# Kernel optimization log

Measured on AMD Instinct MI355X. Metric: run time of the kernel, lower is better.

The kernel has to match this reference:

```python
import jax, jax.numpy as jnp
import numpy as np

B, D, C, P, H, I, E, TOPK = 65536, 1024, 256, 32, 128, 32, 16, 2
FUSION = D + P  # 1056

def ln(x, g, b, eps=1e-5):
    m = jnp.mean(x, axis=-1, keepdims=True)
    v = jnp.mean((x - m) ** 2, axis=-1, keepdims=True)
    return (x - m) * jax.lax.rsqrt(v + eps) * g + b

def setup_inputs() -> dict:
    key = jax.random.key(0)
    ks = jax.random.split(key, 8)
    def w(k, shape):
        return jax.random.normal(k, shape, dtype=jnp.float32) * 0.02
    return {
        "x": jax.random.normal(ks[0], (B, D), dtype=jnp.float32),
        "context": jax.random.normal(ks[1], (B, C), dtype=jnp.float32),
        "en_g": jnp.ones((D,), jnp.float32), "en_b": jnp.zeros((D,), jnp.float32),
        "cn_g": jnp.ones((C,), jnp.float32), "cn_b": jnp.zeros((C,), jnp.float32),
        "cp1_w": w(ks[2], (C, P)), "cp1_b": jnp.zeros((P,), jnp.float32),
        "cp2_w": w(ks[3], (P, P)), "cp2_b": jnp.zeros((P,), jnp.float32),
        "cpn_g": jnp.ones((P,), jnp.float32), "cpn_b": jnp.zeros((P,), jnp.float32),
        "fn_g": jnp.ones((FUSION,), jnp.float32), "fn_b": jnp.zeros((FUSION,), jnp.float32),
        "gp1_w": w(ks[4], (FUSION, H)), "gp1_b": jnp.zeros((H,), jnp.float32),
        "ln1_g": jnp.ones((H,), jnp.float32), "ln1_b": jnp.zeros((H,), jnp.float32),
        "gp2_w": w(ks[5], (H, I)), "gp2_b": jnp.zeros((I,), jnp.float32),
        "ln2_g": jnp.ones((I,), jnp.float32), "ln2_b": jnp.zeros((I,), jnp.float32),
        "gp3_w": w(ks[6], (I, E)), "gp3_b": jnp.zeros((E,), jnp.float32),
    }

def reference(x, context, en_g, en_b, cn_g, cn_b, cp1_w, cp1_b, cp2_w, cp2_b,
              cpn_g, cpn_b, fn_g, fn_b, gp1_w, gp1_b, ln1_g, ln1_b,
              gp2_w, gp2_b, ln2_g, ln2_b, gp3_w, gp3_b):
    gelu = lambda t: jax.nn.gelu(t, approximate=False)  # torch default GELU (erf)
    emb = ln(x, en_g, en_b)                               # [B, D]
    ctx = ln(context, cn_g, cn_b)                         # [B, C]
    cf = gelu(ctx @ cp1_w + cp1_b) @ cp2_w + cp2_b        # [B, P]
    cf = ln(cf, cpn_g, cpn_b)
    fusion = ln(jnp.concatenate([emb, cf], axis=-1), fn_g, fn_b)  # [B, FUSION]
    h = gelu(ln(fusion @ gp1_w + gp1_b, ln1_g, ln1_b))    # [B, H]
    inter = gelu(ln(h @ gp2_w + gp2_b, ln2_g, ln2_b))     # [B, I]
    clean_logits = inter @ gp3_w + gp3_b                  # [B, E]
    # inference path: no noise injection (training=False)
    top_v, top_i = jax.lax.top_k(clean_logits, TOPK)
    combined_weights = jax.nn.softmax(top_v / 1.0, axis=-1)  # temperature=1.0
    return combined_weights, top_i, clean_logits
```

## Files before the change

### kernel.cpp

```cpp
#include <hip/hip_runtime.h>
#include <math.h>

namespace {

using s8v = __attribute__((ext_vector_type(8))) short;
using vf4 = __attribute__((ext_vector_type(4))) float;

constexpr int Bn = 65536;
constexpr int Rn = 64;

constexpr size_t OFF_A1H  = 0;
constexpr size_t OFF_A1M  = 270336;
constexpr size_t OFF_A1L  = 540672;
constexpr size_t OFF_C1H  = 811008;
constexpr size_t OFF_C1M  = 827392;
constexpr size_t OFF_C1L  = 843776;
constexpr size_t OFF_C2H  = 860160;
constexpr size_t OFF_C2M  = 862208;
constexpr size_t OFF_C2L  = 864256;
constexpr size_t OFF_G2H  = 866304;
constexpr size_t OFF_G2M  = 874496;
constexpr size_t OFF_G2L  = 882688;
constexpr size_t OFF_VPK  = 890880;
constexpr size_t OFF_UPK  = 892928;
constexpr size_t OFF_CST  = 893184;
constexpr size_t OFF_VPART= 893216;

__device__ __forceinline__ unsigned short bf16_rn(float f) {
    unsigned u = __float_as_uint(f);
    u += 0x7FFFu + ((u >> 16) & 1u);
    return (unsigned short)(u >> 16);
}
__device__ __forceinline__ float bf16_tof(unsigned short h) {
    return __uint_as_float(((unsigned)h) << 16);
}

union S8U { s8v v; unsigned short u[8]; };
union S8P { s8v v; unsigned u32[4]; };

__device__ __forceinline__ vf4 MFMA(s8v a, s8v b, vf4 c) {
    return __builtin_amdgcn_mfma_f32_16x16x32_bf16(a, b, c, 0, 0, 0);
}

__device__ __forceinline__ void mfma6(vf4& acc, s8v ah, s8v am, s8v al,
                                      s8v bh, s8v bm, s8v bl) {
    acc = MFMA(ah, bh, acc);
    acc = MFMA(ah, bm, acc);
    acc = MFMA(am, bh, acc);
    acc = MFMA(ah, bl, acc);
    acc = MFMA(al, bh, acc);
    acc = MFMA(am, bm, acc);
}

__device__ __forceinline__ void split3(float v, unsigned short& h,
                                       unsigned short& m, unsigned short& l) {
    h = bf16_rn(v);
    const float r = v - bf16_tof(h);
    m = bf16_rn(r);
    const float r2 = r - bf16_tof(m);
    l = bf16_rn(r2);
}

__device__ __forceinline__ void split3x8(const float* vv, s8v& H, s8v& M, s8v& L) {
    S8P h, m, l;
    #pragma unroll
    for (int p = 0; p < 4; ++p) {
        const float lo = vv[2 * p], hi = vv[2 * p + 1];
        unsigned ph, pm, pl;
        asm("v_cvt_pk_bf16_f32 %0, %1, %2" : "=v"(ph) : "v"(lo), "v"(hi));
        const float rlo = lo - __uint_as_float(ph << 16);
        const float rhi = hi - __uint_as_float(ph & 0xFFFF0000u);
        asm("v_cvt_pk_bf16_f32 %0, %1, %2" : "=v"(pm) : "v"(rlo), "v"(rhi));
        const float slo = rlo - __uint_as_float(pm << 16);
        const float shi = rhi - __uint_as_float(pm & 0xFFFF0000u);
        asm("v_cvt_pk_bf16_f32 %0, %1, %2" : "=v"(pl) : "v"(slo), "v"(shi));
        h.u32[p] = ph; m.u32[p] = pm; l.u32[p] = pl;
    }
    H = h.v; M = m.v; L = l.v;
}

__device__ __forceinline__ float gelu_f(float v) {
    return 0.5f * v * (1.0f + erff(v * 0.70710678118654752440f));
}

__device__ __forceinline__ void red16(float& s) {
    s += __shfl_xor(s, 1, 64); s += __shfl_xor(s, 2, 64);
    s += __shfl_xor(s, 4, 64); s += __shfl_xor(s, 8, 64);
}

__global__ void cag_prek1(const float* __restrict__ gp1_w,
                          const float* __restrict__ en_g, const float* __restrict__ en_b,
                          const float* __restrict__ fn_g, const float* __restrict__ fn_b,
                          char* __restrict__ ws)
{
    const int t = threadIdx.x, ch = blockIdx.x;
    s8v* A1h = (s8v*)(ws + OFF_A1H);
    s8v* A1m = (s8v*)(ws + OFF_A1M);
    s8v* A1l = (s8v*)(ws + OFF_A1L);
    float* Vpart = (float*)(ws + OFF_VPART);

    for (int s = t; s < 512; s += 256) {
        const int nt = s >> 6, lane = s & 63;
        const int n = nt * 16 + (lane & 15);
        const int jb = ch * 32 + 8 * (lane >> 4);
        S8U h, m, lo;
        #pragma unroll
        for (int r = 0; r < 8; ++r) {
            const int j = jb + r;
            const float sc = fn_g[j] * (j < 1024 ? en_g[j] : 1.0f);
            const float a = sc * gp1_w[(size_t)j * 128 + n];
            split3(a, h.u[r], m.u[r], lo.u[r]);
        }
        A1h[(ch * 8 + nt) * 64 + lane] = h.v;
        A1m[(ch * 8 + nt) * 64 + lane] = m.v;
        A1l[(ch * 8 + nt) * 64 + lane] = lo.v;
    }
    if (t < 128) {
        float v1 = 0.f, v2 = 0.f, v3 = 0.f, v4 = 0.f;
        for (int jj = 0; jj < 32; ++jj) {
            const int j = ch * 32 + jj;
            const float wv = gp1_w[(size_t)j * 128 + t];
            const float fg = fn_g[j];
            if (j < 1024) { v1 = fmaf(fg * en_g[j], wv, v1); v2 = fmaf(fg * en_b[j], wv, v2); }
            v3 = fmaf(fg, wv, v3);
            v4 = fmaf(fn_b[j], wv, v4);
        }
        float* p = Vpart + ((size_t)ch * 128 + t) * 4;
        p[0] = v1; p[1] = v2; p[2] = v3; p[3] = v4;
    }
}

__global__ void cag_prek2(const float* __restrict__ en_g, const float* __restrict__ en_b,
                          const float* __restrict__ cn_g, const float* __restrict__ cn_b,
                          const float* __restrict__ cp1_w, const float* __restrict__ cp1_b,
                          const float* __restrict__ cp2_w, const float* __restrict__ gp2_w,
                          const float* __restrict__ gp1_b,
                          char* __restrict__ ws)
{
    const int t = threadIdx.x, b = blockIdx.x;
    if (b == 0) {
        const float* Vpart = (const float*)(ws + OFF_VPART);
        float* Vpk = (float*)(ws + OFF_VPK);
        float* cst = (float*)(ws + OFF_CST);
        if (t < 128) {
            float v1 = 0.f, v2 = 0.f, v3 = 0.f, v4 = 0.f;
            for (int ch = 0; ch < 33; ++ch) {
                const float* p = Vpart + ((size_t)ch * 128 + t) * 4;
                v1 += p[0]; v2 += p[1]; v3 += p[2]; v4 += p[3];
            }
            v4 += gp1_b[t];
            float* q = Vpk + t * 4;
            q[0] = v1; q[1] = v2; q[2] = v3; q[3] = v4;
        }
        __shared__ float red[256];
        float part[5] = {0.f, 0.f, 0.f, 0.f, 0.f};
        for (int i = t; i < 1024; i += 256) {
            const float g = en_g[i], bb = en_b[i];
            part[0] += g; part[1] += bb; part[2] += g * g; part[3] += g * bb; part[4] += bb * bb;
        }
        for (int f = 0; f < 5; ++f) {
            red[t] = part[f]; __syncthreads();
            for (int s = 128; s > 0; s >>= 1) { if (t < s) red[t] += red[t + s]; __syncthreads(); }
            if (t == 0) cst[f] = red[0];
            __syncthreads();
        }
    } else if (b == 1) {
        s8v* C1h = (s8v*)(ws + OFF_C1H);
        s8v* C1m = (s8v*)(ws + OFF_C1M);
        s8v* C1l = (s8v*)(ws + OFF_C1L);
        float* up = (float*)(ws + OFF_UPK);
        for (int s = t; s < 8 * 2 * 64; s += 256) {
            const int ks = s >> 7, nt = (s >> 6) & 1, lane = s & 63;
            const int n = nt * 16 + (lane & 15);
            const int kb = ks * 32 + 8 * (lane >> 4);
            S8U h, m, lo;
            #pragma unroll
            for (int r = 0; r < 8; ++r) {
                const int k = kb + r;
                const float a = cn_g[k] * cp1_w[k * 32 + n];
                split3(a, h.u[r], m.u[r], lo.u[r]);
            }
            C1h[(ks * 2 + nt) * 64 + lane] = h.v;
            C1m[(ks * 2 + nt) * 64 + lane] = m.v;
            C1l[(ks * 2 + nt) * 64 + lane] = lo.v;
        }
        if (t < 32) {
            float u1 = 0.f, u2 = 0.f;
            for (int c = 0; c < 256; ++c) {
                u1 = fmaf(cn_g[c], cp1_w[c * 32 + t], u1);
                u2 = fmaf(cn_b[c], cp1_w[c * 32 + t], u2);
            }
            up[2 * t] = u1; up[2 * t + 1] = u2 + cp1_b[t];
        }
    } else if (b == 2) {
        s8v* C2h = (s8v*)(ws + OFF_C2H);
        s8v* C2m = (s8v*)(ws + OFF_C2M);
        s8v* C2l = (s8v*)(ws + OFF_C2L);
        if (t < 128) {
            const int nt = t >> 6, lane = t & 63;
            const int n = nt * 16 + (lane & 15);
            const int kb = 8 * (lane >> 4);
            S8U h, m, lo;
            #pragma unroll
            for (int r = 0; r < 8; ++r) {
                const float a = cp2_w[(kb + r) * 32 + n];
                split3(a, h.u[r], m.u[r], lo.u[r]);
            }
            C2h[nt * 64 + lane] = h.v;
            C2m[nt * 64 + lane] = m.v;
            C2l[nt * 64 + lane] = lo.v;
        }
    } else {
        s8v* G2h = (s8v*)(ws + OFF_G2H);
        s8v* G2m = (s8v*)(ws + OFF_G2M);
        s8v* G2l = (s8v*)(ws + OFF_G2L);
        for (int s = t; s < 4 * 2 * 64; s += 256) {
            const int ks = s >> 7, nt = (s >> 6) & 1, lane = s & 63;
            const int n = nt * 16 + (lane & 15);
            const int kb = ks * 32 + 8 * (lane >> 4);
            S8U h, m, lo;
            #pragma unroll
            for (int r = 0; r < 8; ++r) {
                const float a = gp2_w[(kb + r) * 32 + n];
                split3(a, h.u[r], m.u[r], lo.u[r]);
            }
            G2h[(ks * 2 + nt) * 64 + lane] = h.v;
            G2m[(ks * 2 + nt) * 64 + lane] = m.v;
            G2l[(ks * 2 + nt) * 64 + lane] = lo.v;
        }
    }
}

__global__ __launch_bounds__(256, 4)
void cag_main(const float* __restrict__ x, const float* __restrict__ ctx,
              const float* __restrict__ en_g, const float* __restrict__ en_b,
              const float* __restrict__ cpn_g, const float* __restrict__ cpn_b,
              const float* __restrict__ cp2_b,
              const float* __restrict__ ln1_g, const float* __restrict__ ln1_b,
              const float* __restrict__ gp2_b,
              const float* __restrict__ ln2_g, const float* __restrict__ ln2_b,
              const float* __restrict__ gp3_w, const float* __restrict__ gp3_b,
              const char* __restrict__ ws, float* __restrict__ out)
{
    __shared__ __attribute__((aligned(16))) char smU[64 * 132 * 4];
    __shared__ float s_sc4[64][4];
    __shared__ float part_s[4][64];
    __shared__ float part_s2[4][64];
    __shared__ float s_ln1[64][2];
    __shared__ float s_cfs[64], s_cfs2[64];

    short (*fragA)[4][64][8] = (short(*)[4][64][8])smU;
    float (*cfnbuf)[36] = (float(*)[36])(smU + 12288);
    float (*pbuf)[36]   = (float(*)[36])smU;
    float (*hbuf)[132]  = (float(*)[132])smU;
    float (*ibuf)[36]   = (float(*)[36])smU;
    float (*lbuf)[20]   = (float(*)[20])(smU + 16384);

    const int tid = threadIdx.x;
    const int l = tid & 63, w = tid >> 6;
    const int sg = l >> 4, lr = l & 15;
    const int row0 = blockIdx.x * Rn;

    const s8v* A1h = (const s8v*)(ws + OFF_A1H);
    const s8v* A1m = (const s8v*)(ws + OFF_A1M);
    const s8v* A1l = (const s8v*)(ws + OFF_A1L);
    const s8v* C1h = (const s8v*)(ws + OFF_C1H);
    const s8v* C1m = (const s8v*)(ws + OFF_C1M);
    const s8v* C1l = (const s8v*)(ws + OFF_C1L);
    const s8v* C2h = (const s8v*)(ws + OFF_C2H);
    const s8v* C2m = (const s8v*)(ws + OFF_C2M);
    const s8v* C2l = (const s8v*)(ws + OFF_C2L);
    const s8v* G2h = (const s8v*)(ws + OFF_G2H);
    const s8v* G2m = (const s8v*)(ws + OFF_G2M);
    const s8v* G2l = (const s8v*)(ws + OFF_G2L);
    const float* Vpk = (const float*)(ws + OFF_VPK);
    const float* upk = (const float*)(ws + OFF_UPK);
    const float* cst = (const float*)(ws + OFF_CST);

    {
        const int crow = row0 + 16 * w + lr;
        const float* cb = ctx + (size_t)crow * 256 + 8 * sg;
        float cs = 0.f, cs2 = 0.f;
        vf4 ac0 = {0.f, 0.f, 0.f, 0.f}, ac1 = {0.f, 0.f, 0.f, 0.f};
        #pragma unroll
        for (int ks = 0; ks < 8; ++ks) {
            const float4 a0 = *(const float4*)(cb + ks * 32);
            const float4 a1 = *(const float4*)(cb + ks * 32 + 4);
            const float vv[8] = {a0.x, a0.y, a0.z, a0.w, a1.x, a1.y, a1.z, a1.w};
            #pragma unroll
            for (int j = 0; j < 8; ++j) { cs += vv[j]; cs2 = fmaf(vv[j], vv[j], cs2); }
            s8v ah, am, al;
            split3x8(vv, ah, am, al);
            mfma6(ac0, ah, am, al,
                  C1h[(ks * 2 + 0) * 64 + l], C1m[(ks * 2 + 0) * 64 + l], C1l[(ks * 2 + 0) * 64 + l]);
            mfma6(ac1, ah, am, al,
                  C1h[(ks * 2 + 1) * 64 + l], C1m[(ks * 2 + 1) * 64 + l], C1l[(ks * 2 + 1) * 64 + l]);
        }
        cs += __shfl_xor(cs, 16, 64); cs += __shfl_xor(cs, 32, 64);
        cs2 += __shfl_xor(cs2, 16, 64); cs2 += __shfl_xor(cs2, 32, 64);
        const float cm = cs * (1.f / 256.f);
        const float crr = rsqrtf(cs2 * (1.f / 256.f) - cm * cm + 1e-5f);
        float m_r[4], r_r[4];
        #pragma unroll
        for (int rg = 0; rg < 4; ++rg) {
            const int src = 4 * sg + rg;
            m_r[rg] = __shfl(cm, src, 64);
            r_r[rg] = __shfl(crr, src, 64);
        }
        #pragma unroll
        for (int ntl = 0; ntl < 2; ++ntl) {
            const int c = 16 * ntl + lr;
            const float u1 = upk[2 * c], u2 = upk[2 * c + 1];
            #pragma unroll
            for (int rg = 0; rg < 4; ++rg) {
                const float av = (ntl == 0) ? ac0[rg] : ac1[rg];
                const float a1v = r_r[rg] * av - r_r[rg] * m_r[rg] * u1 + u2;
                pbuf[16 * w + 4 * sg + rg][c] = gelu_f(a1v);
            }
        }
        __syncthreads();
        float pv[8];
        const int prow = 16 * w + lr;
        *(float4*)&pv[0] = *(const float4*)&pbuf[prow][8 * sg];
        *(float4*)&pv[4] = *(const float4*)&pbuf[prow][8 * sg + 4];
        s8v ph, pm_, pl;
        split3x8(pv, ph, pm_, pl);
        vf4 a20 = {0.f, 0.f, 0.f, 0.f}, a21 = {0.f, 0.f, 0.f, 0.f};
        mfma6(a20, ph, pm_, pl, C2h[0 * 64 + l], C2m[0 * 64 + l], C2l[0 * 64 + l]);
        mfma6(a21, ph, pm_, pl, C2h[1 * 64 + l], C2m[1 * 64 + l], C2l[1 * 64 + l]);
        const float cb0 = cp2_b[lr], cb1 = cp2_b[16 + lr];
        const float cg0 = cpn_g[lr], cg1 = cpn_g[16 + lr];
        const float cbb0 = cpn_b[lr], cbb1 = cpn_b[16 + lr];
        __syncthreads();
        #pragma unroll
        for (int rg = 0; rg < 4; ++rg) {
            const float v0 = a20[rg] + cb0, v1 = a21[rg] + cb1;
            float s = v0 + v1, s2 = v0 * v0 + v1 * v1;
            red16(s); red16(s2);
            const float pm = s * (1.f / 32.f);
            const float prs = rsqrtf(s2 * (1.f / 32.f) - pm * pm + 1e-5f);
            const float cn0 = (v0 - pm) * prs * cg0 + cbb0;
            const float cn1 = (v1 - pm) * prs * cg1 + cbb1;
            float t = cn0 + cn1, t2 = cn0 * cn0 + cn1 * cn1;
            red16(t); red16(t2);
            const int rr = 16 * w + 4 * sg + rg;
            if (lr == 0) { s_cfs[rr] = t; s_cfs2[rr] = t2; }
            cfnbuf[rr][lr] = cn0; cfnbuf[rr][16 + lr] = cn1;
        }
    }
    __syncthreads();

    vf4 acc[4][2];
    #pragma unroll
    for (int mt = 0; mt < 4; ++mt) { acc[mt][0] = vf4{0.f,0.f,0.f,0.f}; acc[mt][1] = vf4{0.f,0.f,0.f,0.f}; }

    float Sx = 0.f, Sxx = 0.f, Sxg = 0.f, Sxg2 = 0.f, Sxgb = 0.f, Sq = 0.f;

    const float* xb = x + (size_t)(row0 + 16 * w + lr) * 1024 + 8 * sg;
    const int nt0 = 2 * w;

    float4 xc0 = *(const float4*)(xb);
    float4 xc1 = *(const float4*)(xb + 4);
    float4 xn0, xn1;

    #pragma unroll 1
    for (int ks = 0; ks <= 32; ++ks) {
        const size_t q = (size_t)((ks * 8 + nt0) * 64 + l);
        const s8v B0h = A1h[q],      B0m = A1m[q],      B0l = A1l[q];
        const s8v B1h = A1h[q + 64], B1m = A1m[q + 64], B1l = A1l[q + 64];
        if (ks < 32) {
            const int kb = ks * 32 + 8 * sg;
            const float4 g0 = *(const float4*)(en_g + kb);
            const float4 g1 = *(const float4*)(en_g + kb + 4);
            const float4 e0 = *(const float4*)(en_b + kb);
            const float4 e1 = *(const float4*)(en_b + kb + 4);
            if (ks < 31) {
                xn0 = *(const float4*)(xb + (ks + 1) * 32);
                xn1 = *(const float4*)(xb + (ks + 1) * 32 + 4);
            }
            const float vv[8] = {xc0.x, xc0.y, xc0.z, xc0.w, xc1.x, xc1.y, xc1.z, xc1.w};
            const float gg[8] = {g0.x, g0.y, g0.z, g0.w, g1.x, g1.y, g1.z, g1.w};
            const float ee[8] = {e0.x, e0.y, e0.z, e0.w, e1.x, e1.y, e1.z, e1.w};
            #pragma unroll
            for (int j = 0; j < 8; ++j) {
                const float v = vv[j], g = gg[j], b = ee[j];
                Sx += v; Sxx = fmaf(v, v, Sxx);
                const float t = v * g;
                Sxg += t; Sxg2 = fmaf(t, g, Sxg2); Sxgb = fmaf(t, b, Sxgb); Sq = fmaf(t, t, Sq);
            }
            s8v H, M, L;
            split3x8(vv, H, M, L);
            *(s8v*)&fragA[0][w][l][0] = H;
            *(s8v*)&fragA[1][w][l][0] = M;
            *(s8v*)&fragA[2][w][l][0] = L;
        } else {
            float sx = Sx, sxx = Sxx, sxg = Sxg, sxg2 = Sxg2, sxgb = Sxgb, sq = Sq;
            #define RED2(s) { s += __shfl_xor(s, 16, 64); s += __shfl_xor(s, 32, 64); }
            RED2(sx) RED2(sxx) RED2(sxg) RED2(sxg2) RED2(sxgb) RED2(sq)
            #undef RED2
            const float xm = sx * (1.f / 1024.f);
            const float xvar = sxx * (1.f / 1024.f) - xm * xm;
            const float xr = rsqrtf(xvar + 1e-5f);
            const float xrinv = sqrtf(xvar + 1e-5f);
            const float Gs = cst[0], Bs = cst[1], Sg2c = cst[2], Sgbc = cst[3], Sb2c = cst[4];
            const float Semb = xr * (sxg - xm * Gs) + Bs;
            const float Semb2 = xr * xr * (sq - 2.f * xm * sxg2 + xm * xm * Sg2c)
                              + 2.f * xr * (sxgb - xm * Sgbc) + Sb2c;
            const int rr = 16 * w + lr;
            const float fm = (Semb + s_cfs[rr]) * (1.f / 1056.f);
            const float fvar = (Semb2 + s_cfs2[rr]) * (1.f / 1056.f) - fm * fm;
            const float fr = rsqrtf(fvar + 1e-5f);
            if (sg == 0) {
                s_sc4[rr][0] = fr * xr; s_sc4[rr][1] = -fr * xr * xm;
                s_sc4[rr][2] = fr;      s_sc4[rr][3] = -fr * fm;
            }
            float vv[8];
            *(float4*)&vv[0] = *(const float4*)&cfnbuf[rr][8 * sg];
            *(float4*)&vv[4] = *(const float4*)&cfnbuf[rr][8 * sg + 4];
            #pragma unroll
            for (int j = 0; j < 8; ++j) vv[j] *= xrinv;
            s8v H, M, L;
            split3x8(vv, H, M, L);
            *(s8v*)&fragA[0][w][l][0] = H;
            *(s8v*)&fragA[1][w][l][0] = M;
            *(s8v*)&fragA[2][w][l][0] = L;
        }
        asm volatile("s_waitcnt lgkmcnt(0)\n\ts_barrier" ::: "memory");

        __builtin_amdgcn_s_setprio(1);
        #pragma unroll
        for (int mt = 0; mt < 4; ++mt) {
            const s8v ah = *(const s8v*)&fragA[0][mt][l][0];
            const s8v am = *(const s8v*)&fragA[1][mt][l][0];
            const s8v al = *(const s8v*)&fragA[2][mt][l][0];
            mfma6(acc[mt][0], ah, am, al, B0h, B0m, B0l);
            mfma6(acc[mt][1], ah, am, al, B1h, B1m, B1l);
        }
        __builtin_amdgcn_s_setprio(0);
        asm volatile("s_barrier" ::: "memory");
        xc0 = xn0; xc1 = xn1;
    }

    {
        const int tc0 = 16 * (2 * w) + lr, tc1 = 16 * (2 * w + 1) + lr;
        float4 Vc[2];
        Vc[0] = *(const float4*)&Vpk[tc0 * 4];
        Vc[1] = *(const float4*)&Vpk[tc1 * 4];
        #pragma unroll
        for (int mt = 0; mt < 4; ++mt) {
            #pragma unroll
            for (int rg = 0; rg < 4; ++rg) {
                const float4 sc = *(const float4*)&s_sc4[16 * mt + 4 * sg + rg][0];
                #pragma unroll
                for (int ntl = 0; ntl < 2; ++ntl) {
                    acc[mt][ntl][rg] = sc.x * acc[mt][ntl][rg] + sc.y * Vc[ntl].x
                                     + sc.z * Vc[ntl].y + sc.w * Vc[ntl].z + Vc[ntl].w;
                }
            }
        }
        #pragma unroll
        for (int mt = 0; mt < 4; ++mt) {
            #pragma unroll
            for (int rg = 0; rg < 4; ++rg) {
                const float v0 = acc[mt][0][rg], v1 = acc[mt][1][rg];
                float s = v0 + v1, s2 = v0 * v0 + v1 * v1;
                red16(s); red16(s2);
                if (lr == 0) {
                    const int rr = 16 * mt + 4 * sg + rg;
                    part_s[w][rr] = s; part_s2[w][rr] = s2;
                }
            }
        }
        __syncthreads();
        if (tid < 64) {
            const float s = part_s[0][tid] + part_s[1][tid] + part_s[2][tid] + part_s[3][tid];
            const float s2 = part_s2[0][tid] + part_s2[1][tid] + part_s2[2][tid] + part_s2[3][tid];
            const float mn = s * (1.f / 128.f);
            s_ln1[tid][0] = mn;
            s_ln1[tid][1] = rsqrtf(s2 * (1.f / 128.f) - mn * mn + 1e-5f);
        }
        __syncthreads();
        float g1c[2], b1c[2];
        g1c[0] = ln1_g[tc0]; b1c[0] = ln1_b[tc0];
        g1c[1] = ln1_g[tc1]; b1c[1] = ln1_b[tc1];
        #pragma unroll
        for (int mt = 0; mt < 4; ++mt) {
            #pragma unroll
            for (int rg = 0; rg < 4; ++rg) {
                const int rr = 16 * mt + 4 * sg + rg;
                const float mn = s_ln1[rr][0], rs = s_ln1[rr][1];
                #pragma unroll
                for (int ntl = 0; ntl < 2; ++ntl) {
                    const float hp = gelu_f((acc[mt][ntl][rg] - mn) * rs * g1c[ntl] + b1c[ntl]);
                    hbuf[rr][16 * (2 * w + ntl) + lr] = hp;
                }
            }
        }
        __syncthreads();
    }

    float iv[2][4];
    {
        vf4 aG0 = {0.f, 0.f, 0.f, 0.f}, aG1 = {0.f, 0.f, 0.f, 0.f};
        const int hrow = 16 * w + lr;
        #pragma unroll
        for (int ks = 0; ks < 4; ++ks) {
            float pv[8];
            *(float4*)&pv[0] = *(const float4*)&hbuf[hrow][ks * 32 + 8 * sg];
            *(float4*)&pv[4] = *(const float4*)&hbuf[hrow][ks * 32 + 8 * sg + 4];
            s8v ah, am, al;
            split3x8(pv, ah, am, al);
            mfma6(aG0, ah, am, al,
                  G2h[(ks * 2 + 0) * 64 + l], G2m[(ks * 2 + 0) * 64 + l], G2l[(ks * 2 + 0) * 64 + l]);
            mfma6(aG1, ah, am, al,
                  G2h[(ks * 2 + 1) * 64 + l], G2m[(ks * 2 + 1) * 64 + l], G2l[(ks * 2 + 1) * 64 + l]);
        }
        const float gb0 = gp2_b[lr], gb1 = gp2_b[16 + lr];
        const float lg0 = ln2_g[lr], lg1 = ln2_g[16 + lr];
        const float lb0 = ln2_b[lr], lb1 = ln2_b[16 + lr];
        #pragma unroll
        for (int rg = 0; rg < 4; ++rg) {
            const float v0 = aG0[rg] + gb0, v1 = aG1[rg] + gb1;
            float s = v0 + v1, s2 = v0 * v0 + v1 * v1;
            red16(s); red16(s2);
            const float mn = s * (1.f / 32.f);
            const float rs = rsqrtf(s2 * (1.f / 32.f) - mn * mn + 1e-5f);
            iv[0][rg] = gelu_f((v0 - mn) * rs * lg0 + lb0);
            iv[1][rg] = gelu_f((v1 - mn) * rs * lg1 + lb1);
        }
    }
    __syncthreads();
    #pragma unroll
    for (int rg = 0; rg < 4; ++rg) {
        const int rr = 16 * w + 4 * sg + rg;
        ibuf[rr][lr] = iv[0][rg];
        ibuf[rr][16 + lr] = iv[1][rg];
    }
    __syncthreads();

    {
        const int r = tid >> 2, e4 = (tid & 3) * 4;
        float a0 = 0.f, a1 = 0.f, a2 = 0.f, a3 = 0.f;
        #pragma unroll 4
        for (int qq = 0; qq < 32; ++qq) {
            const float v = ibuf[r][qq];
            const float4 w3 = *(const float4*)(gp3_w + qq * 16 + e4);
            a0 = fmaf(v, w3.x, a0); a1 = fmaf(v, w3.y, a1);
            a2 = fmaf(v, w3.z, a2); a3 = fmaf(v, w3.w, a3);
        }
        const float4 b3 = *(const float4*)(gp3_b + e4);
        const float4 lg = make_float4(a0 + b3.x, a1 + b3.y, a2 + b3.z, a3 + b3.w);
        float* outl = out + (size_t)Bn * 4;
        *(float4*)(outl + (size_t)(row0 + r) * 16 + e4) = lg;
        *(float4*)&lbuf[r][e4] = lg;
    }
    __syncthreads();
    if (tid < 64) {
        float v[16];
        #pragma unroll
        for (int e = 0; e < 4; ++e) *(float4*)&v[e * 4] = *(const float4*)&lbuf[tid][e * 4];
        int i0 = 0; float v0 = v[0];
        #pragma unroll
        for (int e = 1; e < 16; ++e) if (v[e] > v0) { v0 = v[e]; i0 = e; }
        int i1 = -1; float v1 = -3.4e38f;
        #pragma unroll
        for (int e = 0; e < 16; ++e) if (e != i0 && v[e] > v1) { v1 = v[e]; i1 = e; }
        const float e1 = expf(v1 - v0);
        const float inv = 1.0f / (1.0f + e1);
        const size_t g = (size_t)(row0 + tid);
        out[g * 2 + 0] = inv;
        out[g * 2 + 1] = e1 * inv;
        float* outi = out + (size_t)Bn * 2;
        outi[g * 2 + 0] = (float)i0;
        outi[g * 2 + 1] = (float)i1;
    }
}

}

extern "C" void kernel_launch(void* const* d_in, const int* in_sizes, int n_in,
                              void* d_out, int out_size, void* d_ws, size_t ws_size,
                              hipStream_t stream) {
    const float* x     = (const float*)d_in[0];
    const float* ctx   = (const float*)d_in[1];
    const float* en_g  = (const float*)d_in[2];
    const float* en_b  = (const float*)d_in[3];
    const float* cn_g  = (const float*)d_in[4];
    const float* cn_b  = (const float*)d_in[5];
    const float* cp1_w = (const float*)d_in[6];
    const float* cp1_b = (const float*)d_in[7];
    const float* cp2_w = (const float*)d_in[8];
    const float* cp2_b = (const float*)d_in[9];
    const float* cpn_g = (const float*)d_in[10];
    const float* cpn_b = (const float*)d_in[11];
    const float* fn_g  = (const float*)d_in[12];
    const float* fn_b  = (const float*)d_in[13];
    const float* gp1_w = (const float*)d_in[14];
    const float* gp1_b = (const float*)d_in[15];
    const float* ln1_g = (const float*)d_in[16];
    const float* ln1_b = (const float*)d_in[17];
    const float* gp2_w = (const float*)d_in[18];
    const float* gp2_b = (const float*)d_in[19];
    const float* ln2_g = (const float*)d_in[20];
    const float* ln2_b = (const float*)d_in[21];
    const float* gp3_w = (const float*)d_in[22];
    const float* gp3_b = (const float*)d_in[23];

    char* ws = (char*)d_ws;
    hipLaunchKernelGGL(cag_prek1, dim3(33), dim3(256), 0, stream,
                       gp1_w, en_g, en_b, fn_g, fn_b, ws);
    hipLaunchKernelGGL(cag_prek2, dim3(4), dim3(256), 0, stream,
                       en_g, en_b, cn_g, cn_b, cp1_w, cp1_b, cp2_w, gp2_w, gp1_b, ws);
    hipLaunchKernelGGL(cag_main, dim3(Bn / Rn), dim3(256), 0, stream,
                       x, ctx, en_g, en_b, cpn_g, cpn_b, cp2_b,
                       ln1_g, ln1_b, gp2_b, ln2_g, ln2_b, gp3_w, gp3_b,
                       ws, (float*)d_out);
}
```

Before: 198.3 us.

## Give each wave its own rows across all GEMM1 columns, dropping LDS fragment exchange

The first GEMM is repartitioned so each wave computes its own 16 rows across all 8 column tiles, instead of all 64 rows across 2 column tiles. A fragments now stay in registers, which removes the per-k-step LDS stores/loads and the two block barriers. The x loads get a two-step prefetch and B fragment loads are software-pipelined between MFMAs. LN1 statistics are reduced within the wave, dropping the cross-wave partial-sum buffers and a sync. Each wave now loads 4x more B weight data per k-step (8 tiles vs 2) from global/L2 and needs more accumulator registers, which may reduce occupancy.

Measured after the change: 344.2 us. 1.74x slower.

```diff
diff --git a/kernel.cpp b/kernel.cpp
--- a/kernel.cpp
+++ b/kernel.cpp
@@ -244,14 +244,10 @@
 {
     __shared__ __attribute__((aligned(16))) char smU[64 * 132 * 4];
     __shared__ float s_sc4[64][4];
-    __shared__ float part_s[4][64];
-    __shared__ float part_s2[4][64];
-    __shared__ float s_ln1[64][2];
     __shared__ float s_cfs[64], s_cfs2[64];
 
-    short (*fragA)[4][64][8] = (short(*)[4][64][8])smU;
+    float (*pbuf)[36]   = (float(*)[36])smU;
     float (*cfnbuf)[36] = (float(*)[36])(smU + 12288);
-    float (*pbuf)[36]   = (float(*)[36])smU;
     float (*hbuf)[132]  = (float(*)[132])smU;
     float (*ibuf)[36]   = (float(*)[36])smU;
     float (*lbuf)[20]   = (float(*)[20])(smU + 16384);
@@ -350,34 +346,34 @@
     }
     __syncthreads();
 
-    vf4 acc[4][2];
+    vf4 acc[8];
     #pragma unroll
-    for (int mt = 0; mt < 4; ++mt) { acc[mt][0] = vf4{0.f,0.f,0.f,0.f}; acc[mt][1] = vf4{0.f,0.f,0.f,0.f}; }
+    for (int nt = 0; nt < 8; ++nt) acc[nt] = vf4{0.f, 0.f, 0.f, 0.f};
 
     float Sx = 0.f, Sxx = 0.f, Sxg = 0.f, Sxg2 = 0.f, Sxgb = 0.f, Sq = 0.f;
 
     const float* xb = x + (size_t)(row0 + 16 * w + lr) * 1024 + 8 * sg;
-    const int nt0 = 2 * w;
 
     float4 xc0 = *(const float4*)(xb);
     float4 xc1 = *(const float4*)(xb + 4);
-    float4 xn0, xn1;
+    float4 xn0 = *(const float4*)(xb + 32);
+    float4 xn1 = *(const float4*)(xb + 36);
+    float4 xp0, xp1;
+
+    s8v Ah, Am, Al;
+    s8v b0h, b0m, b0l, b1h, b1m, b1l;
 
     #pragma unroll 1
-    for (int ks = 0; ks <= 32; ++ks) {
-        const size_t q = (size_t)((ks * 8 + nt0) * 64 + l);
-        const s8v B0h = A1h[q],      B0m = A1m[q],      B0l = A1l[q];
-        const s8v B1h = A1h[q + 64], B1m = A1m[q + 64], B1l = A1l[q + 64];
-        if (ks < 32) {
-            const int kb = ks * 32 + 8 * sg;
-            const float4 g0 = *(const float4*)(en_g + kb);
-            const float4 g1 = *(const float4*)(en_g + kb + 4);
-            const float4 e0 = *(const float4*)(en_b + kb);
-            const float4 e1 = *(const float4*)(en_b + kb + 4);
-            if (ks < 31) {
-                xn0 = *(const float4*)(xb + (ks + 1) * 32);
-                xn1 = *(const float4*)(xb + (ks + 1) * 32 + 4);
-            }
+    for (int ks = 0; ks < 32; ++ks) {
+        const size_t qb = (size_t)(ks * 8) * 64 + l;
+        b0h = A1h[qb];      b0m = A1m[qb];      b0l = A1l[qb];
+        b1h = A1h[qb + 64]; b1m = A1m[qb + 64]; b1l = A1l[qb + 64];
+        const int kb = ks * 32 + 8 * sg;
+        const float4 g0 = *(const float4*)(en_g + kb);
+        const float4 g1 = *(const float4*)(en_g + kb + 4);
+        const float4 e0 = *(const float4*)(en_b + kb);
+        const float4 e1 = *(const float4*)(en_b + kb + 4);
+        {
             const float vv[8] = {xc0.x, xc0.y, xc0.z, xc0.w, xc1.x, xc1.y, xc1.z, xc1.w};
             const float gg[8] = {g0.x, g0.y, g0.z, g0.w, g1.x, g1.y, g1.z, g1.w};
             const float ee[8] = {e0.x, e0.y, e0.z, e0.w, e1.x, e1.y, e1.z, e1.w};
@@ -388,116 +384,120 @@
                 const float t = v * g;
                 Sxg += t; Sxg2 = fmaf(t, g, Sxg2); Sxgb = fmaf(t, b, Sxgb); Sq = fmaf(t, t, Sq);
             }
-            s8v H, M, L;
-            split3x8(vv, H, M, L);
-            *(s8v*)&fragA[0][w][l][0] = H;
-            *(s8v*)&fragA[1][w][l][0] = M;
-            *(s8v*)&fragA[2][w][l][0] = L;
-        } else {
-            float sx = Sx, sxx = Sxx, sxg = Sxg, sxg2 = Sxg2, sxgb = Sxgb, sq = Sq;
-            #define RED2(s) { s += __shfl_xor(s, 16, 64); s += __shfl_xor(s, 32, 64); }
-            RED2(sx) RED2(sxx) RED2(sxg) RED2(sxg2) RED2(sxgb) RED2(sq)
-            #undef RED2
-            const float xm = sx * (1.f / 1024.f);
-            const float xvar = sxx * (1.f / 1024.f) - xm * xm;
-            const float xr = rsqrtf(xvar + 1e-5f);
-            const float xrinv = sqrtf(xvar + 1e-5f);
-            const float Gs = cst[0], Bs = cst[1], Sg2c = cst[2], Sgbc = cst[3], Sb2c = cst[4];
-            const float Semb = xr * (sxg - xm * Gs) + Bs;
-            const float Semb2 = xr * xr * (sq - 2.f * xm * sxg2 + xm * xm * Sg2c)
-                              + 2.f * xr * (sxgb - xm * Sgbc) + Sb2c;
-            const int rr = 16 * w + lr;
-            const float fm = (Semb + s_cfs[rr]) * (1.f / 1056.f);
-            const float fvar = (Semb2 + s_cfs2[rr]) * (1.f / 1056.f) - fm * fm;
-            const float fr = rsqrtf(fvar + 1e-5f);
-            if (sg == 0) {
-                s_sc4[rr][0] = fr * xr; s_sc4[rr][1] = -fr * xr * xm;
-                s_sc4[rr][2] = fr;      s_sc4[rr][3] = -fr * fm;
-            }
-            float vv[8];
-            *(float4*)&vv[0] = *(const float4*)&cfnbuf[rr][8 * sg];
-            *(float4*)&vv[4] = *(const float4*)&cfnbuf[rr][8 * sg + 4];
-            #pragma unroll
-            for (int j = 0; j < 8; ++j) vv[j] *= xrinv;
-            s8v H, M, L;
-            split3x8(vv, H, M, L);
-            *(s8v*)&fragA[0][w][l][0] = H;
-            *(s8v*)&fragA[1][w][l][0] = M;
-            *(s8v*)&fragA[2][w][l][0] = L;
-        }
-        asm volatile("s_waitcnt lgkmcnt(0)\n\ts_barrier" ::: "memory");
-
-        __builtin_amdgcn_s_setprio(1);
-        #pragma unroll
-        for (int mt = 0; mt < 4; ++mt) {
-            const s8v ah = *(const s8v*)&fragA[0][mt][l][0];
-            const s8v am = *(const s8v*)&fragA[1][mt][l][0];
-            const s8v al = *(const s8v*)&fragA[2][mt][l][0];
-            mfma6(acc[mt][0], ah, am, al, B0h, B0m, B0l);
-            mfma6(acc[mt][1], ah, am, al, B1h, B1m, B1l);
-        }
-        __builtin_amdgcn_s_setprio(0);
-        asm volatile("s_barrier" ::: "memory");
+            split3x8(vv, Ah, Am, Al);
+        }
+        mfma6(acc[0], Ah, Am, Al, b0h, b0m, b0l);
+        b0h = A1h[qb + 128]; b0m = A1m[qb + 128]; b0l = A1l[qb + 128];
+        mfma6(acc[1], Ah, Am, Al, b1h, b1m, b1l);
+        b1h = A1h[qb + 192]; b1m = A1m[qb + 192]; b1l = A1l[qb + 192];
+        mfma6(acc[2], Ah, Am, Al, b0h, b0m, b0l);
+        b0h = A1h[qb + 256]; b0m = A1m[qb + 256]; b0l = A1l[qb + 256];
+        mfma6(acc[3], Ah, Am, Al, b1h, b1m, b1l);
+        b1h = A1h[qb + 320]; b1m = A1m[qb + 320]; b1l = A1l[qb + 320];
+        mfma6(acc[4], Ah, Am, Al, b0h, b0m, b0l);
+        b0h = A1h[qb + 384]; b0m = A1m[qb + 384]; b0l = A1l[qb + 384];
+        mfma6(acc[5], Ah, Am, Al, b1h, b1m, b1l);
+        b1h = A1h[qb + 448]; b1m = A1m[qb + 448]; b1l = A1l[qb + 448];
+        if (ks < 30) {
+            xp0 = *(const float4*)(xb + (ks + 2) * 32);
+            xp1 = *(const float4*)(xb + (ks + 2) * 32 + 4);
+        }
+        mfma6(acc[6], Ah, Am, Al, b0h, b0m, b0l);
+        mfma6(acc[7], Ah, Am, Al, b1h, b1m, b1l);
         xc0 = xn0; xc1 = xn1;
-    }
-
+        xn0 = xp0; xn1 = xp1;
+    }
+
+    float xrinv;
     {
-        const int tc0 = 16 * (2 * w) + lr, tc1 = 16 * (2 * w + 1) + lr;
-        float4 Vc[2];
-        Vc[0] = *(const float4*)&Vpk[tc0 * 4];
-        Vc[1] = *(const float4*)&Vpk[tc1 * 4];
-        #pragma unroll
-        for (int mt = 0; mt < 4; ++mt) {
+        float sx = Sx, sxx = Sxx, sxg = Sxg, sxg2 = Sxg2, sxgb = Sxgb, sq = Sq;
+        #define RED2(s) { s += __shfl_xor(s, 16, 64); s += __shfl_xor(s, 32, 64); }
+        RED2(sx) RED2(sxx) RED2(sxg) RED2(sxg2) RED2(sxgb) RED2(sq)
+        #undef RED2
+        const float xm = sx * (1.f / 1024.f);
+        const float xvar = sxx * (1.f / 1024.f) - xm * xm;
+        const float xr = rsqrtf(xvar + 1e-5f);
+        xrinv = sqrtf(xvar + 1e-5f);
+        const float Gs = cst[0], Bs = cst[1], Sg2c = cst[2], Sgbc = cst[3], Sb2c = cst[4];
+        const float Semb = xr * (sxg - xm * Gs) + Bs;
+        const float Semb2 = xr * xr * (sq - 2.f * xm * sxg2 + xm * xm * Sg2c)
+                          + 2.f * xr * (sxgb - xm * Sgbc) + Sb2c;
+        const int rr = 16 * w + lr;
+        const float fm = (Semb + s_cfs[rr]) * (1.f / 1056.f);
+        const float fvar = (Semb2 + s_cfs2[rr]) * (1.f / 1056.f) - fm * fm;
+        const float fr = rsqrtf(fvar + 1e-5f);
+        if (sg == 0) {
+            s_sc4[rr][0] = fr * xr; s_sc4[rr][1] = -fr * xr * xm;
+            s_sc4[rr][2] = fr;      s_sc4[rr][3] = -fr * fm;
+        }
+    }
+    {
+        const int rr = 16 * w + lr;
+        float vv[8];
+        *(float4*)&vv[0] = *(const float4*)&cfnbuf[rr][8 * sg];
+        *(float4*)&vv[4] = *(const float4*)&cfnbuf[rr][8 * sg + 4];
+        #pragma unroll
+        for (int j = 0; j < 8; ++j) vv[j] *= xrinv;
+        split3x8(vv, Ah, Am, Al);
+        const size_t qb = (size_t)(32 * 8) * 64 + l;
+        b0h = A1h[qb];      b0m = A1m[qb];      b0l = A1l[qb];
+        b1h = A1h[qb + 64]; b1m = A1m[qb + 64]; b1l = A1l[qb + 64];
+        mfma6(acc[0], Ah, Am, Al, b0h, b0m, b0l);
+        b0h = A1h[qb + 128]; b0m = A1m[qb + 128]; b0l = A1l[qb + 128];
+        mfma6(acc[1], Ah, Am, Al, b1h, b1m, b1l);
+        b1h = A1h[qb + 192]; b1m = A1m[qb + 192]; b1l = A1l[qb + 192];
+        mfma6(acc[2], Ah, Am, Al, b0h, b0m, b0l);
+        b0h = A1h[qb + 256]; b0m = A1m[qb + 256]; b0l = A1l[qb + 256];
+        mfma6(acc[3], Ah, Am, Al, b1h, b1m, b1l);
+        b1h = A1h[qb + 320]; b1m = A1m[qb + 320]; b1l = A1l[qb + 320];
+        mfma6(acc[4], Ah, Am, Al, b0h, b0m, b0l);
+        b0h = A1h[qb + 384]; b0m = A1m[qb + 384]; b0l = A1l[qb + 384];
+        mfma6(acc[5], Ah, Am, Al, b1h, b1m, b1l);
+        b1h = A1h[qb + 448]; b1m = A1m[qb + 448]; b1l = A1l[qb + 448];
+        mfma6(acc[6], Ah, Am, Al, b0h, b0m, b0l);
+        mfma6(acc[7], Ah, Am, Al, b1h, b1m, b1l);
+    }
+    __syncthreads();
+
+    {
+        float4 s4[4];
+        #pragma unroll
+        for (int rg = 0; rg < 4; ++rg)
+            s4[rg] = *(const float4*)&s_sc4[16 * w + 4 * sg + rg][0];
+        #pragma unroll
+        for (int nt = 0; nt < 8; ++nt) {
+            const float4 Vc = *(const float4*)&Vpk[(16 * nt + lr) * 4];
             #pragma unroll
             for (int rg = 0; rg < 4; ++rg) {
-                const float4 sc = *(const float4*)&s_sc4[16 * mt + 4 * sg + rg][0];
-                #pragma unroll
-                for (int ntl = 0; ntl < 2; ++ntl) {
-                    acc[mt][ntl][rg] = sc.x * acc[mt][ntl][rg] + sc.y * Vc[ntl].x
-                                     + sc.z * Vc[ntl].y + sc.w * Vc[ntl].z + Vc[ntl].w;
-                }
-            }
-        }
-        #pragma unroll
-        for (int mt = 0; mt < 4; ++mt) {
-            #pragma unroll
-            for (int rg = 0; rg < 4; ++rg) {
-                const float v0 = acc[mt][0][rg], v1 = acc[mt][1][rg];
-                float s = v0 + v1, s2 = v0 * v0 + v1 * v1;
-                red16(s); red16(s2);
-                if (lr == 0) {
-                    const int rr = 16 * mt + 4 * sg + rg;
-                    part_s[w][rr] = s; part_s2[w][rr] = s2;
-                }
-            }
-        }
-        __syncthreads();
-        if (tid < 64) {
-            const float s = part_s[0][tid] + part_s[1][tid] + part_s[2][tid] + part_s[3][tid];
-            const float s2 = part_s2[0][tid] + part_s2[1][tid] + part_s2[2][tid] + part_s2[3][tid];
+                acc[nt][rg] = s4[rg].x * acc[nt][rg] + s4[rg].y * Vc.x
+                            + s4[rg].z * Vc.y + s4[rg].w * Vc.z + Vc.w;
+            }
+        }
+        float g1c[8], b1c[8];
+        #pragma unroll
+        for (int nt = 0; nt < 8; ++nt) {
+            g1c[nt] = ln1_g[16 * nt + lr];
+            b1c[nt] = ln1_b[16 * nt + lr];
+        }
+        #pragma unroll
+        for (int rg = 0; rg < 4; ++rg) {
+            float s = 0.f, s2 = 0.f;
+            #pragma unroll
+            for (int nt = 0; nt < 8; ++nt) {
+                const float v = acc[nt][rg];
+                s += v; s2 = fmaf(v, v, s2);
+            }
+            red16(s); red16(s2);
             const float mn = s * (1.f / 128.f);
-            s_ln1[tid][0] = mn;
-            s_ln1[tid][1] = rsqrtf(s2 * (1.f / 128.f) - mn * mn + 1e-5f);
-        }
-        __syncthreads();
-        float g1c[2], b1c[2];
-        g1c[0] = ln1_g[tc0]; b1c[0] = ln1_b[tc0];
-        g1c[1] = ln1_g[tc1]; b1c[1] = ln1_b[tc1];
-        #pragma unroll
-        for (int mt = 0; mt < 4; ++mt) {
-            #pragma unroll
-            for (int rg = 0; rg < 4; ++rg) {
-                const int rr = 16 * mt + 4 * sg + rg;
-                const float mn = s_ln1[rr][0], rs = s_ln1[rr][1];
-                #pragma unroll
-                for (int ntl = 0; ntl < 2; ++ntl) {
-                    const float hp = gelu_f((acc[mt][ntl][rg] - mn) * rs * g1c[ntl] + b1c[ntl]);
-                    hbuf[rr][16 * (2 * w + ntl) + lr] = hp;
-                }
-            }
-        }
-        __syncthreads();
-    }
+            const float rs = rsqrtf(s2 * (1.f / 128.f) - mn * mn + 1e-5f);
+            #pragma unroll
+            for (int nt = 0; nt < 8; ++nt) {
+                const float hp = gelu_f((acc[nt][rg] - mn) * rs * g1c[nt] + b1c[nt]);
+                hbuf[16 * w + 4 * sg + rg][16 * nt + lr] = hp;
+            }
+        }
+    }
+    __syncthreads();
 
     float iv[2][4];
     {
```
